# Kernel optimization log

Hardware: AMD Instinct MI355X
Metric: run time of the kernel (lower is better)

## Reference

```python
import jax, jax.numpy as jnp
import numpy as np

NARROW = 127.0                      # narrow int8 range [-127, 127]
ACT_SCALE = 6.0 / 127.0             # fixed stand-in for learned ActQuant per-tensor scale
FLOW_SCALE = 3.96875 / 127.0        # ConstFlowQuant: max_val 3.96875, 8-bit narrow


def ste_round(x):
    # straight-through rounding (Brevitas-style)
    return x + jax.lax.stop_gradient(jnp.round(x) - x)


def act_quant(x, scale):
    # per-tensor narrow int8 fake-quant (quantize -> clamp -> dequantize)
    return scale * jnp.clip(ste_round(x / scale), -NARROW, NARROW)


def weight_quant(w):
    # per-tensor stats-based narrow int8 weight fake-quant
    s = jax.lax.stop_gradient(jnp.max(jnp.abs(w))) / NARROW + 1e-12
    return s * jnp.clip(ste_round(w / s), -NARROW, NARROW)


def conv2d(x, w, b, groups=1, pad=0):
    y = jax.lax.conv_general_dilated(
        x, w, window_strides=(1, 1), padding=[(pad, pad), (pad, pad)],
        dimension_numbers=("NCHW", "OIHW", "NCHW"), feature_group_count=groups)
    return y + b[None, :, None, None]


def setup_inputs() -> dict:
    key = jax.random.key(0)
    ks = jax.random.split(key, 12)
    B, H, W = 8, 120, 160
    cor_planes = 4 * (2 * 3 + 1) ** 2  # 196
    return {
        "flow": jax.random.normal(ks[0], (B, 2, H, W), jnp.float32),
        "corr": jax.random.normal(ks[1], (B, cor_planes, H, W), jnp.float32),
        "Wc1": jax.random.normal(ks[2], (96, cor_planes, 1, 1), jnp.float32) * 0.05,
        "bc1": jax.random.normal(ks[3], (96,), jnp.float32) * 0.05,
        "Wf1": jax.random.normal(ks[4], (64, 2, 1, 1), jnp.float32) * 0.05,
        "bf1": jax.random.normal(ks[5], (64,), jnp.float32) * 0.05,
        "Wf2": jax.random.normal(ks[6], (32, 64, 1, 1), jnp.float32) * 0.05,
        "bf2": jax.random.normal(ks[7], (32,), jnp.float32) * 0.05,
        "Wd": jax.random.normal(ks[8], (128, 1, 3, 3), jnp.float32) * 0.05,
        "bd": jax.random.normal(ks[9], (128,), jnp.float32) * 0.05,
        "Wp": jax.random.normal(ks[10], (80, 128, 1, 1), jnp.float32) * 0.05,
        "bp": jax.random.normal(ks[11], (80,), jnp.float32) * 0.05,
    }


def reference(flow, corr, Wc1, bc1, Wf1, bf1, Wf2, bf2, Wd, bd, Wp, bp):
    # convc1: 1x1 quant conv with output ActQuant, then ReLU
    cor = jax.nn.relu(act_quant(conv2d(corr, weight_quant(Wc1), bc1), ACT_SCALE))
    # convf1: 1x1 quant conv (no output quant), ReLU
    flo = jax.nn.relu(conv2d(flow, weight_quant(Wf1), bf1))
    # convf2: input ActQuant, 1x1 conv, output quant (shared with convc1), ReLU
    flo = jax.nn.relu(act_quant(conv2d(act_quant(flo, ACT_SCALE), weight_quant(Wf2), bf2), ACT_SCALE))
    # QuantCat with ConstFlowQuant on inputs and output -> [B,128,H,W]
    cor_flo = act_quant(
        jnp.concatenate([act_quant(cor, FLOW_SCALE), act_quant(flo, FLOW_SCALE)], axis=1),
        FLOW_SCALE)
    # depthwise 3x3 quant conv (groups=128), input ActQuant
    d = conv2d(act_quant(cor_flo, ACT_SCALE), weight_quant(Wd), bd, groups=128, pad=1)
    # pointwise 1x1 quant conv, input ActQuant, ReLU
    out = jax.nn.relu(conv2d(act_quant(d, ACT_SCALE), weight_quant(Wp), bp))
    # final QuantCat(out, flow) with ConstFlowQuant -> [B,82,H,W]
    return act_quant(
        jnp.concatenate([act_quant(out, FLOW_SCALE), act_quant(flow, FLOW_SCALE)], axis=1),
        FLOW_SCALE)
```

## Files before the change

kernel.cpp:

```cpp
#include <hip/hip_runtime.h>
#include <hip/hip_bf16.h>
#include <cstddef>

#define BB   8
#define HH   120
#define WW   160
#define HW   19200
#define NPIX 153600
#define CORC 196

#define AS_  ((float)(6.0/127.0))
#define FS_  0.03125f

#define OFF_WF1 18832
#define OFF_WF2 18960
#define OFF_WD  21008
#define OFF_WPQ_US 44320
#define CFQ_BYTE_OFF 131072

typedef __attribute__((ext_vector_type(8)))  short short8;
typedef __attribute__((ext_vector_type(4)))  float f32x4;

__device__ __forceinline__ float clip127(float x) {
    return fminf(fmaxf(x, -127.f), 127.f);
}

__device__ __forceinline__ unsigned short f2bf(float x) {
    unsigned int u = __float_as_uint(x);
    unsigned int r = (u + 0x7fffu + ((u >> 16) & 1u)) >> 16;
    return (unsigned short)r;
}

__global__ __launch_bounds__(256) void quant_weights(
    const float* __restrict__ Wc1, const float* __restrict__ Wf1,
    const float* __restrict__ Wf2, const float* __restrict__ Wd,
    const float* __restrict__ Wp,  float* __restrict__ ws)
{
    __shared__ float red[256];
    const int t = blockIdx.x;
    const float* src = (t == 0) ? Wc1 : (t == 1) ? Wf1 : (t == 2) ? Wf2 : (t == 3) ? Wd : Wp;
    const int n = (t == 0) ? 18816 : (t == 1) ? 128 : (t == 2) ? 2048 : (t == 3) ? 1152 : 10240;
    const int tid = threadIdx.x;

    float m = 0.f;
    for (int i = tid; i < n; i += 256) m = fmaxf(m, fabsf(src[i]));
    red[tid] = m;
    __syncthreads();
    for (int s = 128; s > 0; s >>= 1) {
        if (tid < s) red[tid] = fmaxf(red[tid], red[tid + s]);
        __syncthreads();
    }
    const float s = red[0] / 127.0f + 1e-12f;

    if (t == 0) {
        unsigned short* bf = (unsigned short*)ws + 32;
        for (int j = tid; j < 21504; j += 256) {
            const int e    = j & 7;
            const int l    = (j >> 3) & 63;
            const int tile = j >> 9;
            const int nt   = tile % 6;
            const int kt   = tile / 6;
            const int out  = nt * 16 + (l & 15);
            const int k    = kt * 32 + ((l >> 4) << 3) + e;
            float q = 0.f;
            if (k < 196) q = clip127(rintf(Wc1[out * 196 + k] / s));
            bf[j] = f2bf(q);
        }
        if (tid == 0) ws[2] = s;
    } else if (t == 4) {
        unsigned short* bf = (unsigned short*)ws + OFF_WPQ_US;
        for (int j = tid; j < 10240; j += 256) {
            const int e    = j & 7;
            const int l    = (j >> 3) & 63;
            const int tile = j >> 9;
            const int nt   = tile % 5;
            const int kt   = tile / 5;
            const int o    = nt * 16 + (l & 15);
            const int k    = kt * 32 + ((l >> 4) << 3) + e;
            const float q  = clip127(rintf(Wp[o * 128 + k] / s));
            bf[j] = f2bf(q);
        }
        if (tid == 0) ws[1] = s;
    } else {
        for (int i = tid; i < n; i += 256) {
            const float q = clip127(rintf(src[i] / s));
            if (t == 1) {
                ws[OFF_WF1 + i] = s * q;
            } else if (t == 2) {
                int o = i / 64, c = i % 64;
                ws[OFF_WF2 + c * 32 + o] = s * q;
            } else {
                ws[OFF_WD + i] = q;
            }
        }
        if (tid == 0 && t == 3) ws[0] = s;
    }
}

#define TSTRIDE 136
__global__ __launch_bounds__(256, 4) void k1_convc1(
    const float* __restrict__ corr, const float* __restrict__ bc1,
    const float* __restrict__ ws,   signed char* __restrict__ cfq)
{
    __shared__ signed char t8[96 * TSTRIDE];

    const int tid = threadIdx.x;
    const int w   = tid >> 6;
    const int l   = tid & 63;
    const int p0  = blockIdx.x * 128;
    const int b   = p0 / HW;
    const int hw0 = p0 % HW;
    const float* cp = corr + (size_t)b * CORC * HW + hw0;

    const int r0   = w * 32 + (l & 15);
    const int koff = (l >> 4) << 3;
    const short8* Bfr = (const short8*)((const unsigned short*)ws + 32);

    f32x4 a00 = {0.f,0.f,0.f,0.f}, a01 = a00, a02 = a00, a03 = a00, a04 = a00, a05 = a00;
    f32x4 a10 = a00, a11 = a00, a12 = a00, a13 = a00, a14 = a00, a15 = a00;

#pragma unroll
    for (int kt = 0; kt < 7; ++kt) {
        short8 h0_, l0_, h1_, l1_;
#pragma unroll
        for (int e = 0; e < 8; ++e) {
            const int c = kt * 32 + koff + e;
            float v0 = 0.f, v1 = 0.f;
            if (c < CORC) {
                const float* pc = cp + (size_t)c * HW;
                v0 = pc[r0];
                v1 = pc[r0 + 16];
            }
            const unsigned short h0 = f2bf(v0);
            const unsigned short h1 = f2bf(v1);
            h0_[e] = (short)h0;
            h1_[e] = (short)h1;
            l0_[e] = (short)f2bf(v0 - __uint_as_float((unsigned int)h0 << 16));
            l1_[e] = (short)f2bf(v1 - __uint_as_float((unsigned int)h1 << 16));
        }
#define NTSTEP(A0, A1, NT)                                                        \
        {   short8 bq = Bfr[((kt) * 6 + (NT)) * 64 + l];                          \
            A0 = __builtin_amdgcn_mfma_f32_16x16x32_bf16(l0_, bq, A0, 0, 0, 0);   \
            A0 = __builtin_amdgcn_mfma_f32_16x16x32_bf16(h0_, bq, A0, 0, 0, 0);   \
            A1 = __builtin_amdgcn_mfma_f32_16x16x32_bf16(l1_, bq, A1, 0, 0, 0);   \
            A1 = __builtin_amdgcn_mfma_f32_16x16x32_bf16(h1_, bq, A1, 0, 0, 0);   }
        NTSTEP(a00, a10, 0) NTSTEP(a01, a11, 1) NTSTEP(a02, a12, 2)
        NTSTEP(a03, a13, 3) NTSTEP(a04, a14, 4) NTSTEP(a05, a15, 5)
#undef NTSTEP
    }

    const float sc1 = ws[2];

#define EPI(ACC, NT, TILE)                                                        \
    {   const int out = (NT) * 16 + (l & 15);                                     \
        const float bias = bc1[out];                                              \
        _Pragma("unroll")                                                         \
        for (int i = 0; i < 4; ++i) {                                             \
            const int prow = w * 32 + (TILE) * 16 + ((l >> 4) << 2) + i;          \
            float v  = fmaf(sc1, ACC[i], bias);                                   \
            float aq = AS_ * clip127(rintf(v / AS_));                             \
            float r  = fmaxf(aq, 0.f);                                            \
            float kk = fminf(rintf(r * 32.f), 127.f);                             \
            float cf = kk * FS_;                                                  \
            float q8 = clip127(rintf(cf / AS_));                                  \
            t8[out * TSTRIDE + prow] = (signed char)(int)q8;                      \
        }                                                                         }
    EPI(a00, 0, 0) EPI(a01, 1, 0) EPI(a02, 2, 0) EPI(a03, 3, 0) EPI(a04, 4, 0) EPI(a05, 5, 0)
    EPI(a10, 0, 1) EPI(a11, 1, 1) EPI(a12, 2, 1) EPI(a13, 3, 1) EPI(a14, 4, 1) EPI(a15, 5, 1)
#undef EPI
    __syncthreads();

#pragma unroll
    for (int r = 0; r < 12; ++r) {
        const int d   = r * 256 + tid;
        const int out = d >> 5;
        const int pd  = d & 31;
        const unsigned int v = *(const unsigned int*)(t8 + out * TSTRIDE + pd * 4);
        *(unsigned int*)(cfq + (size_t)(b * 128 + out) * HW + hw0 + pd * 4) = v;
    }
}

typedef __attribute__((ext_vector_type(16))) float f32x16;
__global__ __launch_bounds__(256) void k1_flo(
    const float* __restrict__ flow, const float* __restrict__ bf1,
    const float* __restrict__ bf2,  const float* __restrict__ ws,
    signed char* __restrict__ cfq)
{
    const int p  = blockIdx.x * 256 + threadIdx.x;
    const int b  = p / HW;
    const int hw = p % HW;

    const float f0 = flow[(size_t)(b * 2) * HW + hw];
    const float f1 = flow[(size_t)(b * 2 + 1) * HW + hw];

    f32x16 a2a, a2b;
#pragma unroll
    for (int j = 0; j < 16; ++j) { a2a[j] = 0.f; a2b[j] = 0.f; }

    for (int c = 0; c < 64; ++c) {
        const float w0 = ws[OFF_WF1 + 2 * c];
        const float w1 = ws[OFF_WF1 + 2 * c + 1];
        float v  = fmaf(f0, w0, fmaf(f1, w1, bf1[c]));
        float r  = fmaxf(v, 0.f);
        float af = AS_ * fminf(rintf(r / AS_), 127.f);
        const float* w2 = ws + OFF_WF2 + c * 32;
#pragma unroll
        for (int j = 0; j < 16; ++j) {
            a2a[j] = fmaf(af, w2[j],      a2a[j]);
            a2b[j] = fmaf(af, w2[16 + j], a2b[j]);
        }
    }

    signed char* op = cfq + (size_t)b * 128 * HW + (size_t)96 * HW + hw;
#define FLOEPI(ACC, BASE)                                                        \
    _Pragma("unroll")                                                            \
    for (int j = 0; j < 16; ++j) {                                               \
        const int o = (BASE) + j;                                                \
        float v  = ACC[j] + bf2[o];                                              \
        float aq = AS_ * clip127(rintf(v / AS_));                                \
        float r  = fmaxf(aq, 0.f);                                               \
        float kk = fminf(rintf(r * 32.f), 127.f);                                \
        float cf = kk * FS_;                                                     \
        float q8 = clip127(rintf(cf / AS_));                                     \
        op[(size_t)o * HW] = (signed char)(int)q8;                               \
    }
    FLOEPI(a2a, 0) FLOEPI(a2b, 16)
#undef FLOEPI
}

#define STG_STRIDE 44
__global__ __launch_bounds__(256) void k2_dwpw(
    const float* __restrict__ flow, const float* __restrict__ bd,
    const float* __restrict__ bp,   const float* __restrict__ ws,
    const signed char* __restrict__ cfq, float* __restrict__ out)
{
    __shared__ signed char stage[4 * 128 * STG_STRIDE];
    __shared__ unsigned short afrag[64 * 136];

    const int tid = threadIdx.x;
    const int bid = blockIdx.x;
    const int b   = bid / 300;
    const int rem = bid % 300;
    const int h0  = (rem / 5) * 2;
    const int w0  = (rem % 5) * 32;

    for (int j = tid; j < 5120; j += 256) {
        const int i   = j % 10;
        const int c   = (j / 10) % 128;
        const int row = j / 1280;
        const int h   = h0 - 1 + row;
        const int wb  = w0 - 4 + 4 * i;
        unsigned int v = 0u;
        if (h >= 0 && h < HH && wb >= 0 && wb <= WW - 4)
            v = *(const unsigned int*)(cfq + ((size_t)(b * 128 + c) * HW + (size_t)h * WW + wb));
        *(unsigned int*)(stage + (row * 128 + c) * STG_STRIDE + i * 4) = v;
    }
    __syncthreads();

    const int c0 = tid & 63;
    const int pg = tid >> 6;
    const float sd = ws[0], sp = ws[1];
    const float ASsd = AS_ * sd;

    float wd0[9], wd1[9];
#pragma unroll
    for (int t9 = 0; t9 < 9; ++t9) {
        wd0[t9] = ws[OFF_WD + c0 * 9 + t9];
        wd1[t9] = ws[OFF_WD + (c0 + 64) * 9 + t9];
    }
    const float bd0 = bd[c0], bd1 = bd[c0 + 64];

#pragma unroll
    for (int pp = 0; pp < 16; ++pp) {
        const int pix = pg * 16 + pp;
        const int r   = pix >> 5;
        const int col = pix & 31;
        float s0 = 0.f, s1 = 0.f;
#pragma unroll
        for (int dy = 0; dy < 3; ++dy) {
            const int rb = (r + dy) * 128;
            const int xb = 3 + col;
#pragma unroll
            for (int dd = 0; dd < 3; ++dd) {
                s0 = fmaf((float)stage[(rb + c0     ) * STG_STRIDE + xb + dd], wd0[dy * 3 + dd], s0);
                s1 = fmaf((float)stage[(rb + c0 + 64) * STG_STRIDE + xb + dd], wd1[dy * 3 + dd], s1);
            }
        }
        const float q0 = clip127(rintf(fmaf(ASsd, s0, bd0) / AS_));
        const float q1 = clip127(rintf(fmaf(ASsd, s1, bd1) / AS_));
        afrag[pix * 136 + c0]      = f2bf(q0);
        afrag[pix * 136 + c0 + 64] = f2bf(q1);
    }
    __syncthreads();

    const int wv = tid >> 6;
    const int l  = tid & 63;
    const unsigned short* A = afrag + (size_t)(wv * 16 + (l & 15)) * 136 + ((l >> 4) << 3);
    const short8* Bfr = (const short8*)((const unsigned short*)ws + OFF_WPQ_US);

    f32x4 pc0 = {0.f,0.f,0.f,0.f}, pc1 = pc0, pc2 = pc0, pc3 = pc0, pc4 = pc0;

#define PTSTEP(ACC, KT, NT)                                                      \
    {   short8 bq = Bfr[((KT) * 5 + (NT)) * 64 + l];                             \
        ACC = __builtin_amdgcn_mfma_f32_16x16x32_bf16(a_, bq, ACC, 0, 0, 0);     }
#pragma unroll
    for (int kt = 0; kt < 4; ++kt) {
        short8 a_ = *(const short8*)(A + kt * 32);
        PTSTEP(pc0, kt, 0) PTSTEP(pc1, kt, 1) PTSTEP(pc2, kt, 2)
        PTSTEP(pc3, kt, 3) PTSTEP(pc4, kt, 4)
    }
#undef PTSTEP

    const float ASsp = AS_ * sp;
    float* ob = out + (size_t)b * 82 * HW;

#define PEPI(ACC, NT)                                                            \
    {   const int o = (NT) * 16 + (l & 15);                                      \
        const float bias = bp[o];                                                \
        _Pragma("unroll")                                                        \
        for (int i = 0; i < 4; ++i) {                                            \
            const int pix = wv * 16 + ((l >> 4) << 2) + i;                       \
            const int hw  = (h0 + (pix >> 5)) * WW + w0 + (pix & 31);            \
            float v = fmaf(ASsp, ACC[i], bias);                                  \
            float r = fmaxf(v, 0.f);                                             \
            float k = fminf(rintf(r * 32.f), 127.f);                             \
            ob[(size_t)o * HW + hw] = k * FS_;                                   \
        }                                                                        }
    PEPI(pc0, 0) PEPI(pc1, 1) PEPI(pc2, 2) PEPI(pc3, 3) PEPI(pc4, 4)
#undef PEPI

    if (tid < 128) {
        const int ch  = tid >> 6;
        const int pix = tid & 63;
        const int hw  = (h0 + (pix >> 5)) * WW + w0 + (pix & 31);
        const float f = flow[(size_t)(b * 2 + ch) * HW + hw];
        const float k = clip127(rintf(f * 32.f));
        ob[(size_t)(80 + ch) * HW + hw] = k * FS_;
    }
}

extern "C" void kernel_launch(void* const* d_in, const int* in_sizes, int n_in,
                              void* d_out, int out_size, void* d_ws, size_t ws_size,
                              hipStream_t stream) {
    const float* flow = (const float*)d_in[0];
    const float* corr = (const float*)d_in[1];
    const float* Wc1  = (const float*)d_in[2];
    const float* bc1  = (const float*)d_in[3];
    const float* Wf1  = (const float*)d_in[4];
    const float* bf1  = (const float*)d_in[5];
    const float* Wf2  = (const float*)d_in[6];
    const float* bf2  = (const float*)d_in[7];
    const float* Wd   = (const float*)d_in[8];
    const float* bd   = (const float*)d_in[9];
    const float* Wp   = (const float*)d_in[10];
    const float* bp   = (const float*)d_in[11];

    float* ws = (float*)d_ws;
    signed char* cfq = (signed char*)d_ws + CFQ_BYTE_OFF;
    float* out = (float*)d_out;

    quant_weights<<<5, 256, 0, stream>>>(Wc1, Wf1, Wf2, Wd, Wp, ws);
    k1_convc1<<<NPIX / 128, 256, 0, stream>>>(corr, bc1, ws, cfq);
    k1_flo<<<NPIX / 256, 256, 0, stream>>>(flow, bf1, bf2, ws, cfq);
    k2_dwpw<<<2400, 256, 0, stream>>>(flow, bd, bp, ws, cfq, out);
}
```

Measured before the change: 159.7 us.

## Software-pipeline corr loads two K-steps ahead in convc1 MFMA loop

New measurement: 163.1 us. +2.2%, slower.

```diff
diff --git a/kernel.cpp b/kernel.cpp
--- a/kernel.cpp
+++ b/kernel.cpp
@@ -98,7 +98,7 @@
 }
 
 #define TSTRIDE 136
-__global__ __launch_bounds__(256, 4) void k1_convc1(
+__global__ __launch_bounds__(256, 2) void k1_convc1(
     const float* __restrict__ corr, const float* __restrict__ bc1,
     const float* __restrict__ ws,   signed char* __restrict__ cfq)
 {
@@ -119,35 +119,60 @@
     f32x4 a00 = {0.f,0.f,0.f,0.f}, a01 = a00, a02 = a00, a03 = a00, a04 = a00, a05 = a00;
     f32x4 a10 = a00, a11 = a00, a12 = a00, a13 = a00, a14 = a00, a15 = a00;
 
-#pragma unroll
-    for (int kt = 0; kt < 7; ++kt) {
-        short8 h0_, l0_, h1_, l1_;
-#pragma unroll
-        for (int e = 0; e < 8; ++e) {
-            const int c = kt * 32 + koff + e;
-            float v0 = 0.f, v1 = 0.f;
-            if (c < CORC) {
-                const float* pc = cp + (size_t)c * HW;
-                v0 = pc[r0];
-                v1 = pc[r0 + 16];
-            }
-            const unsigned short h0 = f2bf(v0);
-            const unsigned short h1 = f2bf(v1);
-            h0_[e] = (short)h0;
-            h1_[e] = (short)h1;
-            l0_[e] = (short)f2bf(v0 - __uint_as_float((unsigned int)h0 << 16));
-            l1_[e] = (short)f2bf(v1 - __uint_as_float((unsigned int)h1 << 16));
-        }
-#define NTSTEP(A0, A1, NT)                                                        \
-        {   short8 bq = Bfr[((kt) * 6 + (NT)) * 64 + l];                          \
-            A0 = __builtin_amdgcn_mfma_f32_16x16x32_bf16(l0_, bq, A0, 0, 0, 0);   \
-            A0 = __builtin_amdgcn_mfma_f32_16x16x32_bf16(h0_, bq, A0, 0, 0, 0);   \
-            A1 = __builtin_amdgcn_mfma_f32_16x16x32_bf16(l1_, bq, A1, 0, 0, 0);   \
-            A1 = __builtin_amdgcn_mfma_f32_16x16x32_bf16(h1_, bq, A1, 0, 0, 0);   }
-        NTSTEP(a00, a10, 0) NTSTEP(a01, a11, 1) NTSTEP(a02, a12, 2)
-        NTSTEP(a03, a13, 3) NTSTEP(a04, a14, 4) NTSTEP(a05, a15, 5)
-#undef NTSTEP
-    }
+    float  tA[16], tB[16], tC[16];
+    short8 bA[6],  bB[6];
+    short8 h0_, l0_, h1_, l1_;
+
+#define AISSUE(BUF, KT)                                                          \
+    {   _Pragma("unroll")                                                        \
+        for (int e = 0; e < 8; ++e) {                                            \
+            const int c = (KT) * 32 + koff + e;                                  \
+            const float* pc = cp + (size_t)c * HW;                               \
+            float v0 = 0.f, v1 = 0.f;                                            \
+            if ((KT) < 6 || c < CORC) { v0 = pc[r0]; v1 = pc[r0 + 16]; }         \
+            BUF[e] = v0; BUF[8 + e] = v1;                                        \
+        }                                                                        }
+
+#define BLOAD(BUF, KT)                                                           \
+    {   _Pragma("unroll")                                                        \
+        for (int nt = 0; nt < 6; ++nt) BUF[nt] = Bfr[((KT) * 6 + nt) * 64 + l];  }
+
+#define CONVERT(BUF)                                                             \
+    {   _Pragma("unroll")                                                        \
+        for (int e = 0; e < 8; ++e) {                                            \
+            const float v0 = BUF[e], v1 = BUF[8 + e];                            \
+            const unsigned short h0 = f2bf(v0);                                  \
+            const unsigned short h1 = f2bf(v1);                                  \
+            h0_[e] = (short)h0; h1_[e] = (short)h1;                              \
+            l0_[e] = (short)f2bf(v0 - __uint_as_float((unsigned int)h0 << 16));  \
+            l1_[e] = (short)f2bf(v1 - __uint_as_float((unsigned int)h1 << 16));  \
+        }                                                                        }
+
+#define MF(NT, A0, A1, BBUF)                                                     \
+    A0 = __builtin_amdgcn_mfma_f32_16x16x32_bf16(l0_, BBUF[NT], A0, 0, 0, 0);    \
+    A0 = __builtin_amdgcn_mfma_f32_16x16x32_bf16(h0_, BBUF[NT], A0, 0, 0, 0);    \
+    A1 = __builtin_amdgcn_mfma_f32_16x16x32_bf16(l1_, BBUF[NT], A1, 0, 0, 0);    \
+    A1 = __builtin_amdgcn_mfma_f32_16x16x32_bf16(h1_, BBUF[NT], A1, 0, 0, 0);
+
+#define MFALL(BBUF)                                                              \
+    MF(0, a00, a10, BBUF) MF(1, a01, a11, BBUF) MF(2, a02, a12, BBUF)            \
+    MF(3, a03, a13, BBUF) MF(4, a04, a14, BBUF) MF(5, a05, a15, BBUF)
+
+    AISSUE(tA, 0)  BLOAD(bA, 0)  AISSUE(tB, 1)
+
+    AISSUE(tC, 2)  BLOAD(bB, 1)  CONVERT(tA)  MFALL(bA)
+    AISSUE(tA, 3)  BLOAD(bA, 2)  CONVERT(tB)  MFALL(bB)
+    AISSUE(tB, 4)  BLOAD(bB, 3)  CONVERT(tC)  MFALL(bA)
+    AISSUE(tC, 5)  BLOAD(bA, 4)  CONVERT(tA)  MFALL(bB)
+    AISSUE(tA, 6)  BLOAD(bB, 5)  CONVERT(tB)  MFALL(bA)
+                   BLOAD(bA, 6)  CONVERT(tC)  MFALL(bB)
+                                 CONVERT(tA)  MFALL(bA)
+
+#undef AISSUE
+#undef BLOAD
+#undef CONVERT
+#undef MF
+#undef MFALL
 
     const float sc1 = ws[2];
 
```

## Stage corr tiles into LDS via async global_load_lds double buffering

Applied to the files above, without the earlier changes.

New measurement: 163.3 us. +2.3%, slower.

```diff
diff --git a/kernel.cpp b/kernel.cpp
--- a/kernel.cpp
+++ b/kernel.cpp
@@ -20,6 +20,7 @@
 
 typedef __attribute__((ext_vector_type(8)))  short short8;
 typedef __attribute__((ext_vector_type(4)))  float f32x4;
+typedef unsigned int u32;
 
 __device__ __forceinline__ float clip127(float x) {
     return fminf(fmaxf(x, -127.f), 127.f);
@@ -98,11 +99,11 @@
 }
 
 #define TSTRIDE 136
-__global__ __launch_bounds__(256, 4) void k1_convc1(
+__global__ __launch_bounds__(256, 3) void k1_convc1(
     const float* __restrict__ corr, const float* __restrict__ bc1,
     const float* __restrict__ ws,   signed char* __restrict__ cfq)
 {
-    __shared__ signed char t8[96 * TSTRIDE];
+    __shared__ __align__(1024) char smem[32768];
 
     const int tid = threadIdx.x;
     const int w   = tid >> 6;
@@ -112,44 +113,70 @@
     const int hw0 = p0 % HW;
     const float* cp = corr + (size_t)b * CORC * HW + hw0;
 
-    const int r0   = w * 32 + (l & 15);
-    const int koff = (l >> 4) << 3;
     const short8* Bfr = (const short8*)((const unsigned short*)ws + 32);
+
+#define STAGE(KT, BASE)                                                               \
+    {   _Pragma("unroll")                                                             \
+        for (int i = 0; i < 4; ++i) {                                                 \
+            const int cl = w * 8 + i * 2;                                             \
+            int ch = (KT) * 32 + cl + (l >> 5);                                       \
+            ch = ch < CORC ? ch : (CORC - 1);                                         \
+            const char* src = (const char*)cp + (size_t)ch * (HW * 4) + ((l & 31) * 16); \
+            u32* dst = (u32*)(smem + (BASE) + cl * 512);                              \
+            __builtin_amdgcn_global_load_lds(                                         \
+                (const __attribute__((address_space(1))) u32*)src,                    \
+                (__attribute__((address_space(3))) u32*)dst, 16, 0, 0);               \
+        }                                                                             }
 
     f32x4 a00 = {0.f,0.f,0.f,0.f}, a01 = a00, a02 = a00, a03 = a00, a04 = a00, a05 = a00;
     f32x4 a10 = a00, a11 = a00, a12 = a00, a13 = a00, a14 = a00, a15 = a00;
 
-#pragma unroll
+    STAGE(0, 0)
+    STAGE(1, 16384)
+    __syncthreads();
+
+    const int pixoff = (w * 32 + (l & 15)) * 4;
+    const int chbase = (l >> 4) << 3;
+
     for (int kt = 0; kt < 7; ++kt) {
+        const int base = (kt & 1) << 14;
+
+        const short8 b0 = Bfr[(kt * 6 + 0) * 64 + l];
+        const short8 b1 = Bfr[(kt * 6 + 1) * 64 + l];
+        const short8 b2 = Bfr[(kt * 6 + 2) * 64 + l];
+        const short8 b3 = Bfr[(kt * 6 + 3) * 64 + l];
+        const short8 b4 = Bfr[(kt * 6 + 4) * 64 + l];
+        const short8 b5 = Bfr[(kt * 6 + 5) * 64 + l];
+
         short8 h0_, l0_, h1_, l1_;
 #pragma unroll
         for (int e = 0; e < 8; ++e) {
-            const int c = kt * 32 + koff + e;
-            float v0 = 0.f, v1 = 0.f;
-            if (c < CORC) {
-                const float* pc = cp + (size_t)c * HW;
-                v0 = pc[r0];
-                v1 = pc[r0 + 16];
-            }
+            const char* ap = smem + base + (chbase + e) * 512 + pixoff;
+            const float v0 = *(const float*)ap;
+            const float v1 = *(const float*)(ap + 64);
             const unsigned short h0 = f2bf(v0);
             const unsigned short h1 = f2bf(v1);
-            h0_[e] = (short)h0;
-            h1_[e] = (short)h1;
+            h0_[e] = (short)h0; h1_[e] = (short)h1;
             l0_[e] = (short)f2bf(v0 - __uint_as_float((unsigned int)h0 << 16));
             l1_[e] = (short)f2bf(v1 - __uint_as_float((unsigned int)h1 << 16));
         }
-#define NTSTEP(A0, A1, NT)                                                        \
-        {   short8 bq = Bfr[((kt) * 6 + (NT)) * 64 + l];                          \
-            A0 = __builtin_amdgcn_mfma_f32_16x16x32_bf16(l0_, bq, A0, 0, 0, 0);   \
-            A0 = __builtin_amdgcn_mfma_f32_16x16x32_bf16(h0_, bq, A0, 0, 0, 0);   \
-            A1 = __builtin_amdgcn_mfma_f32_16x16x32_bf16(l1_, bq, A1, 0, 0, 0);   \
-            A1 = __builtin_amdgcn_mfma_f32_16x16x32_bf16(h1_, bq, A1, 0, 0, 0);   }
-        NTSTEP(a00, a10, 0) NTSTEP(a01, a11, 1) NTSTEP(a02, a12, 2)
-        NTSTEP(a03, a13, 3) NTSTEP(a04, a14, 4) NTSTEP(a05, a15, 5)
-#undef NTSTEP
-    }
+
+#define MF(BB_, A0, A1)                                                          \
+        A0 = __builtin_amdgcn_mfma_f32_16x16x32_bf16(l0_, BB_, A0, 0, 0, 0);     \
+        A0 = __builtin_amdgcn_mfma_f32_16x16x32_bf16(h0_, BB_, A0, 0, 0, 0);     \
+        A1 = __builtin_amdgcn_mfma_f32_16x16x32_bf16(l1_, BB_, A1, 0, 0, 0);     \
+        A1 = __builtin_amdgcn_mfma_f32_16x16x32_bf16(h1_, BB_, A1, 0, 0, 0);
+        MF(b0, a00, a10) MF(b1, a01, a11) MF(b2, a02, a12)
+        MF(b3, a03, a13) MF(b4, a04, a14) MF(b5, a05, a15)
+#undef MF
+
+        __syncthreads();
+        if (kt < 5) STAGE(kt + 2, base)
+    }
+#undef STAGE
 
     const float sc1 = ws[2];
+    signed char* t8 = (signed char*)smem;
 
 #define EPI(ACC, NT, TILE)                                                        \
     {   const int out = (NT) * 16 + (l & 15);                                     \
```

## Stage corr tile through LDS with vectorized loads in convc1

Applied to the files above, without the earlier changes.

New measurement: 168.2 us. 5.3% more time.

```diff
diff --git a/kernel.cpp b/kernel.cpp
--- a/kernel.cpp
+++ b/kernel.cpp
@@ -20,6 +20,7 @@
 
 typedef __attribute__((ext_vector_type(8)))  short short8;
 typedef __attribute__((ext_vector_type(4)))  float f32x4;
+typedef unsigned int u32;
 
 __device__ __forceinline__ float clip127(float x) {
     return fminf(fmaxf(x, -127.f), 127.f);
@@ -97,86 +98,116 @@
     }
 }
 
-#define TSTRIDE 136
-__global__ __launch_bounds__(256, 4) void k1_convc1(
+#define LSTR 225
+#define TS8  36
+__global__ __launch_bounds__(128, 3) void k1_convc1(
     const float* __restrict__ corr, const float* __restrict__ bc1,
     const float* __restrict__ ws,   signed char* __restrict__ cfq)
 {
-    __shared__ signed char t8[96 * TSTRIDE];
+    __shared__ __align__(16) u32 lds[32 * LSTR];
 
     const int tid = threadIdx.x;
     const int w   = tid >> 6;
     const int l   = tid & 63;
-    const int p0  = blockIdx.x * 128;
+    const int p0  = blockIdx.x * 32;
     const int b   = p0 / HW;
     const int hw0 = p0 % HW;
     const float* cp = corr + (size_t)b * CORC * HW + hw0;
 
-    const int r0   = w * 32 + (l & 15);
-    const int koff = (l >> 4) << 3;
     const short8* Bfr = (const short8*)((const unsigned short*)ws + 32);
 
-    f32x4 a00 = {0.f,0.f,0.f,0.f}, a01 = a00, a02 = a00, a03 = a00, a04 = a00, a05 = a00;
-    f32x4 a10 = a00, a11 = a00, a12 = a00, a13 = a00, a14 = a00, a15 = a00;
+    const int lch = tid >> 3;
+    const int px0 = (tid & 7) * 4;
+
+    f32x4 buf[13];
+#pragma unroll
+    for (int r = 0; r < 13; ++r) {
+        const int ch  = r * 16 + lch;
+        const int chc = ch < CORC ? ch : (CORC - 1);
+        buf[r] = *(const f32x4*)(cp + (size_t)chc * HW + px0);
+    }
+
+#pragma unroll
+    for (int r = 0; r < 13; ++r) {
+        const int ch = r * 16 + lch;
+        const bool live = ch < CORC;
+#pragma unroll
+        for (int i = 0; i < 4; ++i) {
+            const float v  = live ? buf[r][i] : 0.f;
+            const unsigned short h = f2bf(v);
+            const float hf = __uint_as_float((u32)h << 16);
+            const unsigned short lo = f2bf(v - hf);
+            lds[(px0 + i) * LSTR + ch] = ((u32)h << 16) | (u32)lo;
+        }
+    }
+#pragma unroll
+    for (int i = 0; i < 4; ++i)
+        lds[(px0 + i) * LSTR + 208 + lch] = 0u;
+    __syncthreads();
+
+    const u32* rowp = lds + (size_t)(w * 16 + (l & 15)) * LSTR;
+    const int  chb  = (l >> 4) << 3;
+    union S8 { short8 s; u32 d[4]; };
+
+    f32x4 ac0 = {0.f,0.f,0.f,0.f}, ac1 = ac0, ac2 = ac0, ac3 = ac0, ac4 = ac0, ac5 = ac0;
 
 #pragma unroll
     for (int kt = 0; kt < 7; ++kt) {
-        short8 h0_, l0_, h1_, l1_;
-#pragma unroll
-        for (int e = 0; e < 8; ++e) {
-            const int c = kt * 32 + koff + e;
-            float v0 = 0.f, v1 = 0.f;
-            if (c < CORC) {
-                const float* pc = cp + (size_t)c * HW;
-                v0 = pc[r0];
-                v1 = pc[r0 + 16];
-            }
-            const unsigned short h0 = f2bf(v0);
-            const unsigned short h1 = f2bf(v1);
-            h0_[e] = (short)h0;
-            h1_[e] = (short)h1;
-            l0_[e] = (short)f2bf(v0 - __uint_as_float((unsigned int)h0 << 16));
-            l1_[e] = (short)f2bf(v1 - __uint_as_float((unsigned int)h1 << 16));
-        }
-#define NTSTEP(A0, A1, NT)                                                        \
-        {   short8 bq = Bfr[((kt) * 6 + (NT)) * 64 + l];                          \
-            A0 = __builtin_amdgcn_mfma_f32_16x16x32_bf16(l0_, bq, A0, 0, 0, 0);   \
-            A0 = __builtin_amdgcn_mfma_f32_16x16x32_bf16(h0_, bq, A0, 0, 0, 0);   \
-            A1 = __builtin_amdgcn_mfma_f32_16x16x32_bf16(l1_, bq, A1, 0, 0, 0);   \
-            A1 = __builtin_amdgcn_mfma_f32_16x16x32_bf16(h1_, bq, A1, 0, 0, 0);   }
-        NTSTEP(a00, a10, 0) NTSTEP(a01, a11, 1) NTSTEP(a02, a12, 2)
-        NTSTEP(a03, a13, 3) NTSTEP(a04, a14, 4) NTSTEP(a05, a15, 5)
-#undef NTSTEP
+        const short8 b0 = Bfr[(kt * 6 + 0) * 64 + l];
+        const short8 b1 = Bfr[(kt * 6 + 1) * 64 + l];
+        const short8 b2 = Bfr[(kt * 6 + 2) * 64 + l];
+        const short8 b3 = Bfr[(kt * 6 + 3) * 64 + l];
+        const short8 b4 = Bfr[(kt * 6 + 4) * 64 + l];
+        const short8 b5 = Bfr[(kt * 6 + 5) * 64 + l];
+
+        u32 pv[8];
+#pragma unroll
+        for (int e = 0; e < 8; ++e) pv[e] = rowp[kt * 32 + chb + e];
+
+        S8 H, L;
+#pragma unroll
+        for (int j = 0; j < 4; ++j) {
+            const u32 a = pv[2 * j], c = pv[2 * j + 1];
+            H.d[j] = (a >> 16) | (c & 0xffff0000u);
+            L.d[j] = (a & 0xffffu) | (c << 16);
+        }
+
+#define MF(BB_, A0)                                                              \
+        A0 = __builtin_amdgcn_mfma_f32_16x16x32_bf16(L.s, BB_, A0, 0, 0, 0);     \
+        A0 = __builtin_amdgcn_mfma_f32_16x16x32_bf16(H.s, BB_, A0, 0, 0, 0);
+        MF(b0, ac0) MF(b1, ac1) MF(b2, ac2) MF(b3, ac3) MF(b4, ac4) MF(b5, ac5)
+#undef MF
     }
 
     const float sc1 = ws[2];
-
-#define EPI(ACC, NT, TILE)                                                        \
+    __syncthreads();
+    signed char* t8 = (signed char*)lds;
+
+#define EPI(ACC, NT)                                                              \
     {   const int out = (NT) * 16 + (l & 15);                                     \
         const float bias = bc1[out];                                              \
         _Pragma("unroll")                                                         \
         for (int i = 0; i < 4; ++i) {                                             \
-            const int prow = w * 32 + (TILE) * 16 + ((l >> 4) << 2) + i;          \
+            const int pix = w * 16 + ((l >> 4) << 2) + i;                         \
             float v  = fmaf(sc1, ACC[i], bias);                                   \
             float aq = AS_ * clip127(rintf(v / AS_));                             \
             float r  = fmaxf(aq, 0.f);                                            \
             float kk = fminf(rintf(r * 32.f), 127.f);                             \
             float cf = kk * FS_;                                                  \
             float q8 = clip127(rintf(cf / AS_));                                  \
-            t8[out * TSTRIDE + prow] = (signed char)(int)q8;                      \
+            t8[out * TS8 + pix] = (signed char)(int)q8;                           \
         }                                                                         }
-    EPI(a00, 0, 0) EPI(a01, 1, 0) EPI(a02, 2, 0) EPI(a03, 3, 0) EPI(a04, 4, 0) EPI(a05, 5, 0)
-    EPI(a10, 0, 1) EPI(a11, 1, 1) EPI(a12, 2, 1) EPI(a13, 3, 1) EPI(a14, 4, 1) EPI(a15, 5, 1)
+    EPI(ac0, 0) EPI(ac1, 1) EPI(ac2, 2) EPI(ac3, 3) EPI(ac4, 4) EPI(ac5, 5)
 #undef EPI
     __syncthreads();
 
 #pragma unroll
-    for (int r = 0; r < 12; ++r) {
-        const int d   = r * 256 + tid;
-        const int out = d >> 5;
-        const int pd  = d & 31;
-        const unsigned int v = *(const unsigned int*)(t8 + out * TSTRIDE + pd * 4);
-        *(unsigned int*)(cfq + (size_t)(b * 128 + out) * HW + hw0 + pd * 4) = v;
+    for (int r = 0; r < 6; ++r) {
+        const int d   = r * 128 + tid;
+        const int out = d >> 3;
+        const int pd  = d & 7;
+        const u32 v = *(const u32*)(t8 + out * TS8 + pd * 4);
+        *(u32*)(cfq + (size_t)(b * 128 + out) * HW + hw0 + pd * 4) = v;
     }
 }
 
@@ -360,7 +391,7 @@
     float* out = (float*)d_out;
 
     quant_weights<<<5, 256, 0, stream>>>(Wc1, Wf1, Wf2, Wd, Wp, ws);
-    k1_convc1<<<NPIX / 128, 256, 0, stream>>>(corr, bc1, ws, cfq);
+    k1_convc1<<<NPIX / 32, 128, 0, stream>>>(corr, bc1, ws, cfq);
     k1_flo<<<NPIX / 256, 256, 0, stream>>>(flow, bf1, bf2, ws, cfq);
     k2_dwpw<<<2400, 256, 0, stream>>>(flow, bd, bp, ws, cfq, out);
 }
```
